# Performance work log

Measured on AMD Instinct MI355X. Metric: run time of the kernel, lower is better.

The kernel has to match this reference:

```python
import jax, jax.numpy as jnp
import numpy as np
from jax import lax

B, S, D = 4, 2048, 256      # batch, seq_len, hidden_dim
F = 1024                    # ffn_dim
E = 32                      # num_experts
K = 4                       # top_k


def setup_inputs() -> dict:
    key = jax.random.key(0)
    ks = jax.random.split(key, 5)
    scale = 0.02
    x = jax.random.normal(ks[0], (B, S, D), dtype=jnp.float32)
    router_w = jax.random.normal(ks[1], (E, D), dtype=jnp.float32) * scale   # gate Linear weight [out=E, in=D]
    w_gate = jax.random.normal(ks[2], (E, F, D), dtype=jnp.float32) * scale  # per-expert [F, D]
    w_up = jax.random.normal(ks[3], (E, F, D), dtype=jnp.float32) * scale
    w_down = jax.random.normal(ks[4], (E, D, F), dtype=jnp.float32) * scale
    return {"x": x, "router_w": router_w, "w_gate": w_gate, "w_up": w_up, "w_down": w_down}


def reference(x, router_w, w_gate, w_up, w_down):
    # Eval mode: jitter noise and dropout are inactive (training-only in the source).
    b, s, d = x.shape
    T = b * s
    xf = x.reshape(T, d)                                   # [T, D]

    # --- Router ---
    logits = xf @ router_w.T                               # [T, E]
    tk_logits, tk_idx = lax.top_k(logits, K)               # [T, K]
    tk_w = jax.nn.softmax(tk_logits, axis=-1)              # [T, K]
    probs = jax.nn.softmax(logits, axis=-1)                # [T, E]
    one_hot = jax.nn.one_hot(tk_idx, E, dtype=x.dtype)     # [T, K, E]
    tokens_per_expert = one_hot.sum(axis=(0, 1))           # [E]
    f_frac = tokens_per_expert / T
    P = probs.mean(axis=0)
    aux_loss = E * (f_frac * P).sum()

    # combine[t, e] = sum_k tk_w[t,k] * [tk_idx[t,k] == e]
    combine = jnp.einsum("tk,tke->te", tk_w, one_hot)      # [T, E]

    # --- Experts: scan over experts, SwiGLU FFN, weighted accumulate ---
    def step(acc, params):
        wg, wu, wd, ce = params                            # [F,D], [F,D], [D,F], [T]
        h = jax.nn.silu(xf @ wg.T) * (xf @ wu.T)           # [T, F]
        return acc + ce[:, None] * (h @ wd.T), None

    out, _ = lax.scan(step, jnp.zeros_like(xf),
                      (w_gate, w_up, w_down, combine.T))
    return out.reshape(b, s, d), aux_loss
```

## Files before the change

kernel.cpp:

```cpp
#include <hip/hip_runtime.h>
#include <math.h>

#define TOK 8192
#define DIM 256
#define NE  32
#define NK  4
#define NF  1024

typedef __bf16 bf16x8 __attribute__((ext_vector_type(8)));
typedef float  f32x4  __attribute__((ext_vector_type(4)));
typedef unsigned short u16x8 __attribute__((ext_vector_type(8)));

__device__ __forceinline__ unsigned short f2b(float f) {
  unsigned u = __builtin_bit_cast(unsigned, f);
  unsigned r = (u + 0x7FFFu + ((u >> 16) & 1u)) >> 16;
  return (unsigned short)r;
}

__device__ __forceinline__ void gload16(const void* g, void* l) {
  __builtin_amdgcn_global_load_lds(
      (const __attribute__((address_space(1))) void*)g,
      (__attribute__((address_space(3))) void*)l, 16, 0, 0);
}

__global__ __launch_bounds__(256) void router_kernel(
    const float* __restrict__ x, const float* __restrict__ rw,
    int* __restrict__ counts, float* __restrict__ psum,
    int* __restrict__ etok, float* __restrict__ ewt,
    float* __restrict__ outz)
{
  __shared__ float xs[32][DIM + 4];
  __shared__ float ws[NE][DIM + 4];
  __shared__ float lg[32][NE];
  __shared__ int hist[NE];
  __shared__ int base[NE];

  const int tid = threadIdx.x;
  const int t0 = blockIdx.x * 32;

  {
    float4 z4 = {0.f, 0.f, 0.f, 0.f};
    float4* og = (float4*)(outz + (size_t)t0 * DIM);
    #pragma unroll
    for (int i = 0; i < 8; i++) og[i*256 + tid] = z4;
  }

  {
    const float4* xg = (const float4*)(x + (size_t)t0 * DIM);
    for (int i = tid; i < 32 * (DIM/4); i += 256) {
      int t = i / (DIM/4), c = i % (DIM/4);
      *(float4*)&xs[t][c*4] = xg[t*(DIM/4)+c];
    }
    const float4* wgp = (const float4*)rw;
    for (int i = tid; i < NE * (DIM/4); i += 256) {
      int e = i / (DIM/4), c = i % (DIM/4);
      *(float4*)&ws[e][c*4] = wgp[e*(DIM/4)+c];
    }
  }
  if (tid < NE) hist[tid] = 0;
  __syncthreads();

  for (int i = 0; i < 4; i++) {
    int idx = i*256 + tid;
    int t = idx >> 5, e = idx & 31;
    float acc = 0.f;
    for (int c = 0; c < DIM/4; c++) {
      float4 a = *(const float4*)&xs[t][c*4];
      float4 b = *(const float4*)&ws[e][c*4];
      acc += a.x*b.x + a.y*b.y + a.z*b.z + a.w*b.w;
    }
    lg[t][e] = acc;
  }
  __syncthreads();

  int ids[NK]; int slots[NK]; float wts[NK];
  if (tid < 32) {
    const int t = tid;
    float l[NE];
    #pragma unroll
    for (int e = 0; e < NE; e++) l[e] = lg[t][e];
    unsigned mask = 0;
    float vals[NK];
    #pragma unroll
    for (int k = 0; k < NK; k++) {
      float best = -INFINITY; int bi = 0;
      for (int e = 0; e < NE; e++)
        if (!((mask >> e) & 1u) && l[e] > best) { best = l[e]; bi = e; }
      mask |= 1u << bi; vals[k] = best; ids[k] = bi;
    }
    float s4 = 0.f;
    #pragma unroll
    for (int k = 0; k < NK; k++) { wts[k] = __expf(vals[k] - vals[0]); s4 += wts[k]; }
    #pragma unroll
    for (int k = 0; k < NK; k++) wts[k] /= s4;
    float s = 0.f;
    for (int e = 0; e < NE; e++) { l[e] = __expf(l[e] - vals[0]); s += l[e]; }
    float inv = 1.f / s;
    for (int e = 0; e < NE; e++) lg[t][e] = l[e] * inv;
    #pragma unroll
    for (int k = 0; k < NK; k++) slots[k] = atomicAdd(&hist[ids[k]], 1);
  }
  __syncthreads();
  if (tid < NE) {
    float s = 0.f;
    for (int t = 0; t < 32; t++) s += lg[t][tid];
    atomicAdd(&psum[tid], s);
    int h = hist[tid];
    base[tid] = h ? atomicAdd(&counts[tid], h) : 0;
  }
  __syncthreads();
  if (tid < 32) {
    #pragma unroll
    for (int k = 0; k < NK; k++) {
      int p = base[ids[k]] + slots[k];
      etok[(size_t)ids[k]*TOK + p] = t0 + tid;
      ewt [(size_t)ids[k]*TOK + p] = wts[k];
    }
  }
}

#define CVT_TOTAL (NE * 96 * 1024)
#define CVT_BLOCKS 2048

__global__ __launch_bounds__(256) void convert_kernel(
    const float* __restrict__ wg_, const float* __restrict__ wu_,
    const float* __restrict__ wd_, unsigned short* __restrict__ wB)
{
  int gid = blockIdx.x * 256 + threadIdx.x;
  #pragma unroll 1
  for (; gid < CVT_TOTAL; gid += CVT_BLOCKS * 256) {
    int sg  = gid >> 10;
    int idx = gid & 1023;
    int e   = sg / 96;
    int st  = sg - e * 96;
    int ch  = st / 3;
    int ty  = st - ch * 3;
    unsigned short* dst = wB + ((size_t)sg << 13);
    const float* src;
    int pos;
    if (ty < 2) {
      int f = idx >> 5, gk = idx & 31;
      const float* w = (ty == 0) ? wg_ : wu_;
      src = w + (size_t)e * (NF*DIM) + (size_t)(ch*32 + f) * DIM + (gk << 3);
      pos = f*256 + ((gk ^ (f & 7)) << 3);
    } else {
      int d = idx >> 2, fg = idx & 3;
      src = wd_ + (size_t)e * (DIM*NF) + (size_t)d * NF + (ch << 5) + (fg << 3);
      pos = (d << 5) + ((fg ^ ((d >> 1) & 3)) << 3);
    }
    float4 a = *(const float4*)src;
    float4 c = *(const float4*)(src + 4);
    u16x8 v;
    v[0]=f2b(a.x); v[1]=f2b(a.y); v[2]=f2b(a.z); v[3]=f2b(a.w);
    v[4]=f2b(c.x); v[5]=f2b(c.y); v[6]=f2b(c.z); v[7]=f2b(c.w);
    *(u16x8*)&dst[pos] = v;
  }
}

__global__ void aux_kernel(const int* __restrict__ counts,
                           const float* __restrict__ psum,
                           float* __restrict__ aux_out)
{
  int tid = threadIdx.x;
  float v = 0.f;
  if (tid < NE) v = (counts[tid] / (float)TOK) * (psum[tid] / (float)TOK);
  #pragma unroll
  for (int off = 32; off; off >>= 1) v += __shfl_down(v, off);
  if (tid == 0) aux_out[0] = (float)NE * v;
}

#define PWB(N) asm volatile("s_waitcnt vmcnt(" #N ") lgkmcnt(0)\n\ts_barrier" ::: "memory")

#define ISSUE_L(sl_) do {                                               \
    const unsigned short* sp_ = wE + ((size_t)(3*c0 + (sl_)) << 13);    \
    unsigned short* dp_ = &ring[(sl_) & 3][0];                          \
    _Pragma("unroll")                                                   \
    for (int i_ = 0; i_ < 2; i_++) {                                    \
      int o_ = (i_*512 + tid) << 3;                                     \
      gload16(sp_ + o_, dp_ + o_);                                      \
    }                                                                   \
  } while (0)

#define COMP_G(rs)                                                      \
  { const int fl = nw*16 + ln;                                          \
    const int rowb = fl*256, xo = fl & 7;                               \
    ga = (f32x4){0,0,0,0};                                              \
    _Pragma("unroll")                                                   \
    for (int kk = 0; kk < 8; kk++) {                                    \
      bf16x8 bg = *(const bf16x8*)&rs[rowb + (((kk*4 + q) ^ xo) << 3)]; \
      ga = __builtin_amdgcn_mfma_f32_16x16x32_bf16(xf[kk], bg, ga, 0,0,0); \
    } }

#define COMP_U(rs)                                                      \
  { const int fl = nw*16 + ln;                                          \
    const int rowb = fl*256, xo = fl & 7;                               \
    f32x4 ua = (f32x4){0,0,0,0};                                        \
    _Pragma("unroll")                                                   \
    for (int kk = 0; kk < 8; kk++) {                                    \
      bf16x8 bu = *(const bf16x8*)&rs[rowb + (((kk*4 + q) ^ xo) << 3)]; \
      ua = __builtin_amdgcn_mfma_f32_16x16x32_bf16(xf[kk], bu, ua, 0,0,0); \
    }                                                                   \
    const int fu = fl >> 3, f7 = fl & 7;                                \
    _Pragma("unroll")                                                   \
    for (int rr = 0; rr < 4; rr++) {                                    \
      const int row = mw*16 + q*4 + rr;                                 \
      float g0 = ga[rr];                                                \
      hs[row*32 + (((fu ^ ((row >> 1) & 3)) << 3) | f7)] =              \
          f2b((g0 / (1.f + __expf(-g0))) * ua[rr]);                     \
    } }

#define COMP_D(rs)                                                      \
  { const int arow = mw*16 + ln;                                        \
    bf16x8 a = *(const bf16x8*)&hs[arow*32 + ((q ^ ((arow >> 1) & 3)) << 3)]; \
    _Pragma("unroll")                                                   \
    for (int nt = 0; nt < 8; nt++) {                                    \
      const int d = nw*128 + nt*16 + ln;                                \
      bf16x8 bd = *(const bf16x8*)&rs[d*32 + ((q ^ ((d >> 1) & 3)) << 3)]; \
      oacc[nt] = __builtin_amdgcn_mfma_f32_16x16x32_bf16(a, bd, oacc[nt], 0,0,0); \
    } }

__global__ __launch_bounds__(512, 4) void expert_mfma11_kernel(
    const float* __restrict__ x,
    const unsigned short* __restrict__ wB,
    const int* __restrict__ counts,
    const int* __restrict__ etok, const float* __restrict__ ewt,
    float* __restrict__ out)
{
  __shared__ unsigned short ring[4][8192];
  __shared__ unsigned short hs[2048];
  __shared__ int   lel[64];
  __shared__ float lwt[64];
  __shared__ int   pfx[NE + 1];

  const int tid  = threadIdx.x;
  const int lane = tid & 63;
  const int wv   = tid >> 6;
  const int mw   = wv & 3;
  const int nw   = wv >> 2;
  const int q    = lane >> 4;
  const int ln   = lane & 15;

  if (tid == 0) {
    int acc = 0;
    #pragma unroll 1
    for (int e = 0; e < NE; e++) { pfx[e] = acc; acc += (counts[e] + 63) >> 6; }
    pfx[NE] = acc;
  }
  __syncthreads();

  const int U  = __builtin_amdgcn_readfirstlane(pfx[NE] << 5);
  const int ub = ((blockIdx.x & 7) << 6) | (blockIdx.x >> 3);
  int       u  = (ub * U) >> 9;
  const int u1 = ((ub + 1) * U) >> 9;

  #pragma unroll 1
  while (u < u1) {
    const int g = u >> 5;
    int ev = 0;
    #pragma unroll 1
    while (pfx[ev + 1] <= g) ev++;
    const int e   = __builtin_amdgcn_readfirstlane(ev);
    const int t   = __builtin_amdgcn_readfirstlane(g - pfx[e]);
    const int c0  = u & 31;
    const int c1  = (32 < c0 + (u1 - u)) ? 32 : (c0 + (u1 - u));
    const int cnt = __builtin_amdgcn_readfirstlane(counts[e]);
    const int t0  = t << 6;
    const unsigned short* wE = wB + (size_t)e * 96 * 8192;
    const int*   el = etok + (size_t)e * TOK;
    const float* ew = ewt  + (size_t)e * TOK;

    if (tid < 64) {
      int gt = t0 + tid;
      lel[tid] = (gt < cnt) ? el[gt] : -1;
      lwt[tid] = (gt < cnt) ? ew[gt] : 0.f;
    }
    __syncthreads();

    bf16x8 xf[8];
    {
      int row = mw*16 + ln;
      int tok = lel[row]; if (tok < 0) tok = 0;
      const float* xr = x + (size_t)tok * DIM;
      #pragma unroll
      for (int k = 0; k < 8; k++) {
        float4 a = *(const float4*)(xr + k*32 + q*8);
        float4 c = *(const float4*)(xr + k*32 + q*8 + 4);
        union { bf16x8 v; unsigned short s[8]; } tt;
        tt.s[0]=f2b(a.x); tt.s[1]=f2b(a.y); tt.s[2]=f2b(a.z); tt.s[3]=f2b(a.w);
        tt.s[4]=f2b(c.x); tt.s[5]=f2b(c.y); tt.s[6]=f2b(c.z); tt.s[7]=f2b(c.w);
        xf[k] = tt.v;
      }
    }

    f32x4 oacc[8];
    #pragma unroll
    for (int nt = 0; nt < 8; nt++) oacc[nt] = (f32x4){0,0,0,0};

    const int S = 3 * (c1 - c0);

    asm volatile("s_waitcnt vmcnt(0)" ::: "memory");
    ISSUE_L(0); ISSUE_L(1); ISSUE_L(2);

    f32x4 ga;

    #pragma unroll 1
    for (int c = c0; c < c1; c++) {
      const int sb = 3 * (c - c0);
      PWB(2);
      if (sb + 3 < S) ISSUE_L(sb + 3);
      { const unsigned short* rs = ring[ sb      & 3]; COMP_G(rs); }
      { const unsigned short* rs = ring[(sb + 1) & 3]; COMP_U(rs); }
      if (sb + 3 < S) {
        PWB(2);
        ISSUE_L(sb + 4);
        ISSUE_L(sb + 5);
      } else {
        PWB(0);
      }
      { const unsigned short* rs = ring[(sb + 2) & 3]; COMP_D(rs); }
    }

    #pragma unroll
    for (int nt = 0; nt < 8; nt++) {
      int d = nw*128 + nt*16 + ln;
      #pragma unroll
      for (int rr = 0; rr < 4; rr++) {
        int tl = mw*16 + q*4 + rr;
        int tok = lel[tl];
        if (tok >= 0)
          atomicAdd(&out[(size_t)tok*DIM + d], lwt[tl] * oacc[nt][rr]);
      }
    }
    __syncthreads();

    u += c1 - c0;
  }
}

__global__ __launch_bounds__(512, 2) void expert_mfma5_kernel(
    const float* __restrict__ x,
    const float* __restrict__ wg_, const float* __restrict__ wu_,
    const float* __restrict__ wd_,
    const int* __restrict__ counts,
    const int* __restrict__ etok, const float* __restrict__ ewt,
    float* __restrict__ out)
{
  const int b  = blockIdx.x;
  const int j  = b >> 3;
  const int e  = (b & 7) + 8 * (j & 3);
  const int s0 = j >> 2;
  const int cnt = counts[e];

  __shared__ unsigned short stg[2][16384];
  __shared__ unsigned short hsf[128][72];
  __shared__ int   lel[128];
  __shared__ float lwt[128];

  const int tid  = threadIdx.x;
  const int lane = tid & 63;
  const int wv   = tid >> 6;
  const int mw   = wv & 3;
  const int nw   = wv >> 2;
  const int q    = lane >> 4;
  const int ln   = lane & 15;

  int guOff[4], dOff[4], dRow[4], dFg[4];
  #pragma unroll
  for (int i = 0; i < 4; i++) {
    int G = i*512 + tid;
    int f = G >> 5, gk = G & 31;
    guOff[i] = f*256 + ((gk ^ (f & 7)) << 3);
    int d = G >> 3, fg = G & 7;
    dOff[i] = d*64 + ((fg ^ (d & 7)) << 3);
    dRow[i] = d; dFg[i] = fg;
  }

  const float* wgE = wg_ + (size_t)e * NF * DIM;
  const float* wuE = wu_ + (size_t)e * NF * DIM;
  const float* wdE = wd_ + (size_t)e * DIM * NF;

  const int*   el = etok + (size_t)e * TOK;
  const float* ew = ewt  + (size_t)e * TOK;

  for (int t0 = s0 * 128; t0 < cnt; t0 += 1024) {
    if (tid < 128) {
      int gt = t0 + tid;
      lel[tid] = (gt < cnt) ? el[gt] : -1;
      lwt[tid] = (gt < cnt) ? ew[gt] : 0.f;
    }
    __syncthreads();

    bf16x8 xf[2][8];
    #pragma unroll
    for (int m = 0; m < 2; m++) {
      int row = mw*32 + m*16 + ln;
      int tok = lel[row]; if (tok < 0) tok = 0;
      const float* xr = x + (size_t)tok * DIM;
      #pragma unroll
      for (int k = 0; k < 8; k++) {
        float4 a = *(const float4*)(xr + k*32 + q*8);
        float4 c = *(const float4*)(xr + k*32 + q*8 + 4);
        union { bf16x8 v; unsigned short s[8]; } t;
        t.s[0]=f2b(a.x); t.s[1]=f2b(a.y); t.s[2]=f2b(a.z); t.s[3]=f2b(a.w);
        t.s[4]=f2b(c.x); t.s[5]=f2b(c.y); t.s[6]=f2b(c.z); t.s[7]=f2b(c.w);
        xf[m][k] = t.v;
      }
    }

    f32x4 oacc[8][2];
    #pragma unroll
    for (int nt = 0; nt < 8; nt++) { oacc[nt][0] = (f32x4){0,0,0,0}; oacc[nt][1] = (f32x4){0,0,0,0}; }

    unsigned short* pA = stg[0];
    unsigned short* pB = stg[1];
    float4 r[8];

    {
      const float4* s4 = (const float4*)wgE;
      #pragma unroll
      for (int i = 0; i < 4; i++) { int G = i*512 + tid; r[2*i] = s4[2*G]; r[2*i+1] = s4[2*G+1]; }
      #pragma unroll
      for (int i = 0; i < 4; i++) {
        u16x8 v;
        v[0]=f2b(r[2*i].x);   v[1]=f2b(r[2*i].y);   v[2]=f2b(r[2*i].z);   v[3]=f2b(r[2*i].w);
        v[4]=f2b(r[2*i+1].x); v[5]=f2b(r[2*i+1].y); v[6]=f2b(r[2*i+1].z); v[7]=f2b(r[2*i+1].w);
        *(u16x8*)&pA[guOff[i]] = v;
      }
    }
    __syncthreads();

    f32x4 ga[2][2];

    for (int ch = 0; ch < 16; ch++) {
      {
        const float4* s4 = (const float4*)(wuE + (size_t)ch*16384);
        #pragma unroll
        for (int i = 0; i < 4; i++) { int G = i*512 + tid; r[2*i] = s4[2*G]; r[2*i+1] = s4[2*G+1]; }
      }
      #pragma unroll
      for (int nt = 0; nt < 2; nt++) {
        int fl = nw*32 + nt*16 + ln;
        int rowb = fl*256, xo = fl & 7;
        ga[nt][0] = (f32x4){0,0,0,0}; ga[nt][1] = (f32x4){0,0,0,0};
        #pragma unroll
        for (int kk = 0; kk < 8; kk++) {
          bf16x8 bg = *(const bf16x8*)&pA[rowb + (((kk*4 + q) ^ xo) << 3)];
          ga[nt][0] = __builtin_amdgcn_mfma_f32_16x16x32_bf16(xf[0][kk], bg, ga[nt][0], 0,0,0);
          ga[nt][1] = __builtin_amdgcn_mfma_f32_16x16x32_bf16(xf[1][kk], bg, ga[nt][1], 0,0,0);
        }
      }
      #pragma unroll
      for (int i = 0; i < 4; i++) {
        u16x8 v;
        v[0]=f2b(r[2*i].x);   v[1]=f2b(r[2*i].y);   v[2]=f2b(r[2*i].z);   v[3]=f2b(r[2*i].w);
        v[4]=f2b(r[2*i+1].x); v[5]=f2b(r[2*i+1].y); v[6]=f2b(r[2*i+1].z); v[7]=f2b(r[2*i+1].w);
        *(u16x8*)&pB[guOff[i]] = v;
      }
      __syncthreads();
      { unsigned short* t = pA; pA = pB; pB = t; }

      {
        #pragma unroll
        for (int i = 0; i < 4; i++) {
          const float4* p = (const float4*)(wdE + (size_t)dRow[i]*NF + ch*64 + dFg[i]*8);
          r[2*i] = p[0]; r[2*i+1] = p[1];
        }
      }
      #pragma unroll
      for (int nt = 0; nt < 2; nt++) {
        int fl = nw*32 + nt*16 + ln;
        int rowb = fl*256, xo = fl & 7;
        f32x4 ua0 = (f32x4){0,0,0,0}, ua1 = (f32x4){0,0,0,0};
        #pragma unroll
        for (int kk = 0; kk < 8; kk++) {
          bf16x8 bu = *(const bf16x8*)&pA[rowb + (((kk*4 + q) ^ xo) << 3)];
          ua0 = __builtin_amdgcn_mfma_f32_16x16x32_bf16(xf[0][kk], bu, ua0, 0,0,0);
          ua1 = __builtin_amdgcn_mfma_f32_16x16x32_bf16(xf[1][kk], bu, ua1, 0,0,0);
        }
        #pragma unroll
        for (int rr = 0; rr < 4; rr++) {
          float g0 = ga[nt][0][rr], g1 = ga[nt][1][rr];
          hsf[mw*32      + q*4 + rr][fl] = f2b((g0 / (1.f + __expf(-g0))) * ua0[rr]);
          hsf[mw*32 + 16 + q*4 + rr][fl] = f2b((g1 / (1.f + __expf(-g1))) * ua1[rr]);
        }
      }
      #pragma unroll
      for (int i = 0; i < 4; i++) {
        u16x8 v;
        v[0]=f2b(r[2*i].x);   v[1]=f2b(r[2*i].y);   v[2]=f2b(r[2*i].z);   v[3]=f2b(r[2*i].w);
        v[4]=f2b(r[2*i+1].x); v[5]=f2b(r[2*i+1].y); v[6]=f2b(r[2*i+1].z); v[7]=f2b(r[2*i+1].w);
        *(u16x8*)&pB[dOff[i]] = v;
      }
      __syncthreads();
      { unsigned short* t = pA; pA = pB; pB = t; }

      if (ch < 15) {
        const float4* s4 = (const float4*)(wgE + (size_t)(ch+1)*16384);
        #pragma unroll
        for (int i = 0; i < 4; i++) { int G = i*512 + tid; r[2*i] = s4[2*G]; r[2*i+1] = s4[2*G+1]; }
      }
      #pragma unroll
      for (int kk = 0; kk < 2; kk++) {
        bf16x8 a0 = *(const bf16x8*)&hsf[mw*32      + ln][kk*32 + q*8];
        bf16x8 a1 = *(const bf16x8*)&hsf[mw*32 + 16 + ln][kk*32 + q*8];
        #pragma unroll
        for (int nt = 0; nt < 8; nt++) {
          int d = nw*128 + nt*16 + ln;
          bf16x8 bd = *(const bf16x8*)&pA[d*64 + (((kk*4 + q) ^ (d & 7)) << 3)];
          oacc[nt][0] = __builtin_amdgcn_mfma_f32_16x16x32_bf16(a0, bd, oacc[nt][0], 0,0,0);
          oacc[nt][1] = __builtin_amdgcn_mfma_f32_16x16x32_bf16(a1, bd, oacc[nt][1], 0,0,0);
        }
      }
      if (ch < 15) {
        #pragma unroll
        for (int i = 0; i < 4; i++) {
          u16x8 v;
          v[0]=f2b(r[2*i].x);   v[1]=f2b(r[2*i].y);   v[2]=f2b(r[2*i].z);   v[3]=f2b(r[2*i].w);
          v[4]=f2b(r[2*i+1].x); v[5]=f2b(r[2*i+1].y); v[6]=f2b(r[2*i+1].z); v[7]=f2b(r[2*i+1].w);
          *(u16x8*)&pB[guOff[i]] = v;
        }
      }
      __syncthreads();
      { unsigned short* t = pA; pA = pB; pB = t; }
    }

    #pragma unroll
    for (int nt = 0; nt < 8; nt++) {
      int d = nw*128 + nt*16 + ln;
      #pragma unroll
      for (int m = 0; m < 2; m++)
        #pragma unroll
        for (int rr = 0; rr < 4; rr++) {
          int tl = mw*32 + m*16 + q*4 + rr;
          int tok = lel[tl];
          if (tok >= 0)
            atomicAdd(&out[(size_t)tok*DIM + d], lwt[tl] * oacc[nt][m][rr]);
        }
    }
    __syncthreads();
  }
}

extern "C" void kernel_launch(void* const* d_in, const int* in_sizes, int n_in,
                              void* d_out, int out_size, void* d_ws, size_t ws_size,
                              hipStream_t stream)
{
  const float* x  = (const float*)d_in[0];
  const float* rw = (const float*)d_in[1];
  const float* wg = (const float*)d_in[2];
  const float* wu = (const float*)d_in[3];
  const float* wd = (const float*)d_in[4];
  float* out = (float*)d_out;

  int*   counts = (int*)d_ws;
  float* psum   = (float*)((char*)d_ws + 128);
  int*   etok   = (int*)((char*)d_ws + 256);
  float* ewt    = (float*)((char*)d_ws + 256 + (size_t)NE*TOK*4);

  hipMemsetAsync(d_ws, 0, 256, stream);

  const size_t wboff = (size_t)4 << 20;
  const size_t wbsz  = (size_t)NE * 96 * 8192 * 2;
  if (ws_size >= wboff + wbsz) {
    unsigned short* wB = (unsigned short*)((char*)d_ws + wboff);
    convert_kernel<<<CVT_BLOCKS, 256, 0, stream>>>(wg, wu, wd, wB);
    router_kernel<<<TOK/32, 256, 0, stream>>>(x, rw, counts, psum, etok, ewt, out);
    aux_kernel<<<1, 64, 0, stream>>>(counts, psum, out + (size_t)TOK*DIM);
    expert_mfma11_kernel<<<512, 512, 0, stream>>>(x, wB, counts, etok, ewt, out);
  } else {
    router_kernel<<<TOK/32, 256, 0, stream>>>(x, rw, counts, psum, etok, ewt, out);
    aux_kernel<<<1, 64, 0, stream>>>(counts, psum, out + (size_t)TOK*DIM);
    expert_mfma5_kernel<<<256, 512, 0, stream>>>(x, wg, wu, wd, counts, etok, ewt, out);
  }
}
```

Baseline: 298.3 us.

## Use k-group-major LDS layouts and a three-slot weight ring in expert kernel

Replaces the XOR-swizzled weight and hidden-activation layouts with k-group-major layouts, so each group of 16 lanes reads contiguous 16-byte chunks. The convert kernel now writes weights in this new order. The weight ring shrinks from four slots to three, each tied to a fixed stage (gate, up, down), and loads are re-interleaved. The launch-bounds occupancy hint goes from 4 to 6. This is meant to cut shared-memory use, which allows more resident blocks, and to simplify addressing; the cost is a shallower prefetch pipeline that can expose load latency.

```diff
diff --git a/kernel.cpp b/kernel.cpp
--- a/kernel.cpp
+++ b/kernel.cpp
@@ -139,14 +139,14 @@
     const float* src;
     int pos;
     if (ty < 2) {
-      int f = idx >> 5, gk = idx & 31;
+      int f = idx >> 5, kg = idx & 31;
       const float* w = (ty == 0) ? wg_ : wu_;
-      src = w + (size_t)e * (NF*DIM) + (size_t)(ch*32 + f) * DIM + (gk << 3);
-      pos = f*256 + ((gk ^ (f & 7)) << 3);
+      src = w + (size_t)e * (NF*DIM) + (size_t)(ch*32 + f) * DIM + (kg << 3);
+      pos = (kg*32 + f) << 3;
     } else {
-      int d = idx >> 2, fg = idx & 3;
-      src = wd_ + (size_t)e * (DIM*NF) + (size_t)d * NF + (ch << 5) + (fg << 3);
-      pos = (d << 5) + ((fg ^ ((d >> 1) & 3)) << 3);
+      int d = idx >> 2, kg = idx & 3;
+      src = wd_ + (size_t)e * (DIM*NF) + (size_t)d * NF + (ch << 5) + (kg << 3);
+      pos = (kg*256 + d) << 3;
     }
     float4 a = *(const float4*)src;
     float4 c = *(const float4*)(src + 4);
@@ -173,7 +173,7 @@
 
 #define ISSUE_L(sl_) do {                                               \
     const unsigned short* sp_ = wE + ((size_t)(3*c0 + (sl_)) << 13);    \
-    unsigned short* dp_ = &ring[(sl_) & 3][0];                          \
+    unsigned short* dp_ = &ring[(sl_) % 3][0];                          \
     _Pragma("unroll")                                                   \
     for (int i_ = 0; i_ < 2; i_++) {                                    \
       int o_ = (i_*512 + tid) << 3;                                     \
@@ -183,50 +183,47 @@
 
 #define COMP_G(rs)                                                      \
   { const int fl = nw*16 + ln;                                          \
-    const int rowb = fl*256, xo = fl & 7;                               \
     ga = (f32x4){0,0,0,0};                                              \
     _Pragma("unroll")                                                   \
     for (int kk = 0; kk < 8; kk++) {                                    \
-      bf16x8 bg = *(const bf16x8*)&rs[rowb + (((kk*4 + q) ^ xo) << 3)]; \
+      bf16x8 bg = *(const bf16x8*)&rs[((kk*4 + q)*32 + fl) << 3];       \
       ga = __builtin_amdgcn_mfma_f32_16x16x32_bf16(xf[kk], bg, ga, 0,0,0); \
     } }
 
 #define COMP_U(rs)                                                      \
   { const int fl = nw*16 + ln;                                          \
-    const int rowb = fl*256, xo = fl & 7;                               \
     f32x4 ua = (f32x4){0,0,0,0};                                        \
     _Pragma("unroll")                                                   \
     for (int kk = 0; kk < 8; kk++) {                                    \
-      bf16x8 bu = *(const bf16x8*)&rs[rowb + (((kk*4 + q) ^ xo) << 3)]; \
+      bf16x8 bu = *(const bf16x8*)&rs[((kk*4 + q)*32 + fl) << 3];       \
       ua = __builtin_amdgcn_mfma_f32_16x16x32_bf16(xf[kk], bu, ua, 0,0,0); \
     }                                                                   \
-    const int fu = fl >> 3, f7 = fl & 7;                                \
     _Pragma("unroll")                                                   \
     for (int rr = 0; rr < 4; rr++) {                                    \
       const int row = mw*16 + q*4 + rr;                                 \
       float g0 = ga[rr];                                                \
-      hs[row*32 + (((fu ^ ((row >> 1) & 3)) << 3) | f7)] =              \
+      hs[(((fl >> 3)*64 + row) << 3) | (fl & 7)] =                      \
           f2b((g0 / (1.f + __expf(-g0))) * ua[rr]);                     \
     } }
 
 #define COMP_D(rs)                                                      \
   { const int arow = mw*16 + ln;                                        \
-    bf16x8 a = *(const bf16x8*)&hs[arow*32 + ((q ^ ((arow >> 1) & 3)) << 3)]; \
+    bf16x8 a = *(const bf16x8*)&hs[(q*64 + arow) << 3];                 \
     _Pragma("unroll")                                                   \
     for (int nt = 0; nt < 8; nt++) {                                    \
       const int d = nw*128 + nt*16 + ln;                                \
-      bf16x8 bd = *(const bf16x8*)&rs[d*32 + ((q ^ ((d >> 1) & 3)) << 3)]; \
+      bf16x8 bd = *(const bf16x8*)&rs[(q*256 + d) << 3];                \
       oacc[nt] = __builtin_amdgcn_mfma_f32_16x16x32_bf16(a, bd, oacc[nt], 0,0,0); \
     } }
 
-__global__ __launch_bounds__(512, 4) void expert_mfma11_kernel(
+__global__ __launch_bounds__(512, 6) void expert_mfma12_kernel(
     const float* __restrict__ x,
     const unsigned short* __restrict__ wB,
     const int* __restrict__ counts,
     const int* __restrict__ etok, const float* __restrict__ ewt,
     float* __restrict__ out)
 {
-  __shared__ unsigned short ring[4][8192];
+  __shared__ unsigned short ring[3][8192];
   __shared__ unsigned short hs[2048];
   __shared__ int   lel[64];
   __shared__ float lwt[64];
@@ -299,7 +296,7 @@
     const int S = 3 * (c1 - c0);
 
     asm volatile("s_waitcnt vmcnt(0)" ::: "memory");
-    ISSUE_L(0); ISSUE_L(1); ISSUE_L(2);
+    ISSUE_L(0); ISSUE_L(1);
 
     f32x4 ga;
 
@@ -307,17 +304,18 @@
     for (int c = c0; c < c1; c++) {
       const int sb = 3 * (c - c0);
       PWB(2);
+      ISSUE_L(sb + 2);
+      { const unsigned short* rs = ring[0]; COMP_G(rs); }
+      PWB(2);
       if (sb + 3 < S) ISSUE_L(sb + 3);
-      { const unsigned short* rs = ring[ sb      & 3]; COMP_G(rs); }
-      { const unsigned short* rs = ring[(sb + 1) & 3]; COMP_U(rs); }
+      { const unsigned short* rs = ring[1]; COMP_U(rs); }
       if (sb + 3 < S) {
         PWB(2);
         ISSUE_L(sb + 4);
-        ISSUE_L(sb + 5);
       } else {
         PWB(0);
       }
-      { const unsigned short* rs = ring[(sb + 2) & 3]; COMP_D(rs); }
+      { const unsigned short* rs = ring[2]; COMP_D(rs); }
     }
 
     #pragma unroll
@@ -566,7 +564,7 @@
     convert_kernel<<<CVT_BLOCKS, 256, 0, stream>>>(wg, wu, wd, wB);
     router_kernel<<<TOK/32, 256, 0, stream>>>(x, rw, counts, psum, etok, ewt, out);
     aux_kernel<<<1, 64, 0, stream>>>(counts, psum, out + (size_t)TOK*DIM);
-    expert_mfma11_kernel<<<512, 512, 0, stream>>>(x, wB, counts, etok, ewt, out);
+    expert_mfma12_kernel<<<512, 512, 0, stream>>>(x, wB, counts, etok, ewt, out);
   } else {
     router_kernel<<<TOK/32, 256, 0, stream>>>(x, rw, counts, psum, etok, ewt, out);
     aux_kernel<<<1, 64, 0, stream>>>(counts, psum, out + (size_t)TOK*DIM);
```

New measurement: 332.1 us. +11.3%, slower.
